# Optimization experiments

Hardware: AMD Instinct MI355X
Metric: run time of the kernel (lower is better)

The kernel has to match this reference:

```python
import jax, jax.numpy as jnp
import numpy as np

K = 16
ITERS = 5
DIST_CHUNK = 8  # feature-chunk size to avoid materializing [B,F,S,S]


def pairwise_l1(x):
    """x: [B, F, S] -> d: [B, S, S], d[b,i,j] = ||x[b,:,i]-x[b,:,j]||_1.
    Computed in feature chunks via scan so peak intermediate is [B,CH,S,S]."""
    B, F, S = x.shape
    xc = x.reshape(B, F // DIST_CHUNK, DIST_CHUNK, S).transpose(1, 0, 2, 3)  # [F/CH,B,CH,S]

    def step(acc, blk):  # blk: [B, CH, S]
        return acc + jnp.abs(blk[:, :, :, None] - blk[:, :, None, :]).sum(axis=1), None

    d, _ = jax.lax.scan(step, jnp.zeros((B, S, S), x.dtype), xc)
    return d


def kmedoids_pool(x, w):
    B, F, S = x.shape
    wm = jnp.mean(w, axis=1)                       # [B,S] per-token attention weight
    d = pairwise_l1(x)                             # [B,S,S]
    _, ctr = jax.lax.top_k(wm, K)                  # [B,K] initial medoids
    dw = d * wm[:, None, :]                        # d[b,i,j]*w[b,j]
    for _ in range(ITERS):
        # distance from every token to each current medoid: [B,S,K]
        i2c = jnp.take_along_axis(d, jnp.broadcast_to(ctr[:, None, :], (B, S, K)), axis=2)
        assign = jnp.argmin(i2c, axis=2)           # [B,S] cluster assignment
        member = jax.nn.one_hot(assign, K, dtype=x.dtype)  # [B,S,K]
        # weighted within-cluster cost for candidate i in cluster k:
        # cost[b,i,k] = sum_j d[b,i,j]*w[b,j]*member[b,j,k]
        cost = jnp.einsum('bij,bjk->bik', dw, member)
        cost = jnp.where(member > 0, cost, jnp.inf)  # medoid must be a member
        ctr = jnp.argmin(cost, axis=1)             # [B,K] new medoids
    idx = jnp.broadcast_to(ctr[:, None, :], (B, F, K))
    return jnp.take_along_axis(x, idx, axis=2)     # [B,F,K]


def setup_inputs() -> dict:
    key = jax.random.key(0)
    kx, kw = jax.random.split(key)
    B, F, S = 8, 256, 1024
    x = jax.random.normal(kx, (B, F, S), dtype=jnp.float32)
    w = jax.random.uniform(kw, (B, S, S), dtype=jnp.float32)
    return {"x": x, "w": w}


def reference(x, w):
    return kmedoids_pool(x, w)
```

## Files before the change

kernel.cpp:

```cpp
#include <hip/hip_runtime.h>
#include <math.h>

#define BB 8
#define FF 256
#define SS 1024
#define KK 16
#define ITERS 5

typedef unsigned long long ull;


#define ICH 8
__global__ void wm_part_kernel(const float* __restrict__ w, float* __restrict__ part) {
    int j = blockIdx.x * 256 + threadIdx.x;
    int ic = blockIdx.y, b = blockIdx.z;
    const float* wp = w + (size_t)b * SS * SS + (size_t)ic * (SS / ICH) * SS + j;
    float s = 0.f;
#pragma unroll 16
    for (int i = 0; i < SS / ICH; ++i) s += wp[(size_t)i * SS];
    part[((size_t)ic * BB + b) * SS + j] = s;
}

#define FCD 8
#define TS 64
#define NT (SS / TS)
__device__ __forceinline__ void async_copy16(const float* g, const float* s) {
    __builtin_amdgcn_global_load_lds((const __attribute__((address_space(1))) void*)g,
                                     (__attribute__((address_space(3))) void*)s, 16, 0, 0);
}

__global__ __launch_bounds__(128, 2) void dist_kernel(const float* __restrict__ x,
                                                      float* __restrict__ d) {
    __shared__ float smem[4096];
    int tid = threadIdx.x;
    int wave = tid >> 6, lane = tid & 63;
    int b = blockIdx.y;
    int w = blockIdx.x * 2 + wave;
    int it = 0, rem = w;
    while (rem >= NT - it) { rem -= NT - it; ++it; }
    int jt = it + rem;
    int i0 = it * TS, j0 = jt * TS;
    const float* xb = x + (size_t)b * FF * SS;
    float* db = d + (size_t)b * SS * SS;
    float* wbase = smem + wave * 2048;
    int ly = lane >> 3, lx = lane & 7;
    int sFl = lane >> 4, sTk = (lane & 15) * 4;

    float acc[8][8] = {};

    auto stage = [&](int c, int h) {
        float* A = wbase + h * 1024;
        const float* base = xb + ((size_t)c * FCD + sFl) * SS;
        async_copy16(base + i0 + sTk, A);
        async_copy16(base + 4 * SS + i0 + sTk, A + 256);
        async_copy16(base + j0 + sTk, A + 512);
        async_copy16(base + 4 * SS + j0 + sTk, A + 768);
    };
    auto compute = [&](int h) {
        const float* A = wbase + h * 1024;
        const float* B = A + 512;
#pragma unroll
        for (int f = 0; f < FCD; ++f) {
            float4 a0 = *(const float4*)(A + f * 64 + ly * 8);
            float4 a1 = *(const float4*)(A + f * 64 + ly * 8 + 4);
            float4 b0 = *(const float4*)(B + f * 64 + lx * 8);
            float4 b1 = *(const float4*)(B + f * 64 + lx * 8 + 4);
            float av[8] = {a0.x, a0.y, a0.z, a0.w, a1.x, a1.y, a1.z, a1.w};
            float bv[8] = {b0.x, b0.y, b0.z, b0.w, b1.x, b1.y, b1.z, b1.w};
#pragma unroll
            for (int r = 0; r < 8; ++r)
#pragma unroll
                for (int c = 0; c < 8; ++c)
                    acc[r][c] += fabsf(av[r] - bv[c]);
        }
    };

    stage(0, 0);
#pragma unroll 1
    for (int k = 0; k < FF / FCD - 1; ++k) {
        asm volatile("s_waitcnt lgkmcnt(0)" ::: "memory");
        stage(k + 1, (k + 1) & 1);
        asm volatile("s_waitcnt vmcnt(4)" ::: "memory");
        compute(k & 1);
    }
    asm volatile("s_waitcnt vmcnt(0)" ::: "memory");
    compute(1);

#pragma unroll
    for (int r = 0; r < 8; ++r) {
        float4 v0 = make_float4(acc[r][0], acc[r][1], acc[r][2], acc[r][3]);
        float4 v1 = make_float4(acc[r][4], acc[r][5], acc[r][6], acc[r][7]);
        float* row = &db[(size_t)(i0 + ly * 8 + r) * SS + j0 + lx * 8];
        *(float4*)row = v0;
        *(float4*)(row + 4) = v1;
    }
    if (it != jt) {
#pragma unroll
        for (int c = 0; c < 8; ++c) {
            float4 v0 = make_float4(acc[0][c], acc[1][c], acc[2][c], acc[3][c]);
            float4 v1 = make_float4(acc[4][c], acc[5][c], acc[6][c], acc[7][c]);
            float* row = &db[(size_t)(j0 + lx * 8 + c) * SS + i0 + ly * 8];
            *(float4*)row = v0;
            *(float4*)(row + 4) = v1;
        }
    }
}

__global__ __launch_bounds__(1024) void topk_assign_kernel(const float* __restrict__ part,
                                                           float* __restrict__ wm,
                                                           const float* __restrict__ d,
                                                           int* __restrict__ assign) {
    int b = blockIdx.x;
    int tid = threadIdx.x;
    int lane = tid & 63, wv = tid >> 6;
    __shared__ ull red[16];
    __shared__ int ctr_s[KK];
    float v = 0.f;
#pragma unroll
    for (int ic = 0; ic < ICH; ++ic) v += part[((size_t)ic * BB + b) * SS + tid];
    v *= (1.0f / SS);
    wm[b * SS + tid] = v;
    ull key = (((ull)__float_as_uint(v)) << 32) | (ull)(0xFFFFFFFFu - (unsigned)tid);
    for (int k = 0; k < KK; ++k) {
        ull kk = key;
#pragma unroll
        for (int off = 32; off; off >>= 1) {
            ull o = __shfl_down(kk, off, 64);
            if (o > kk) kk = o;
        }
        if (lane == 0) red[wv] = kk;
        __syncthreads();
        if (wv == 0) {
            ull k2 = (lane < 16) ? red[lane] : 0ull;
#pragma unroll
            for (int off = 8; off; off >>= 1) {
                ull o = __shfl_down(k2, off, 64);
                if (o > k2) k2 = o;
            }
            if (lane == 0) red[0] = k2;
        }
        __syncthreads();
        ull W = red[0];
        int widx = (int)(0xFFFFFFFFu - (unsigned)(W & 0xFFFFFFFFu));
        if (tid == widx) key = 0;
        if (tid == 0) ctr_s[k] = widx;
        __syncthreads();
    }
    const float* db = d + (size_t)b * SS * SS;
    float bv = INFINITY;
    int bk = 0;
#pragma unroll
    for (int k = 0; k < KK; ++k) {
        float vv = db[(size_t)ctr_s[k] * SS + tid];
        if (vv < bv) { bv = vv; bk = k; }
    }
    assign[b * SS + tid] = bk;
}

#define RPB 16
__global__ __launch_bounds__(256) void cost_kernel(const float* __restrict__ d,
                                                   const float* __restrict__ wm,
                                                   const int* __restrict__ assign,
                                                   float* __restrict__ cost) {
    int b = blockIdx.y;
    int tid = threadIdx.x;
    int lane = tid & 63, wv = tid >> 6;
    __shared__ float wmv[SS];
    __shared__ int asg[SS];
    *(float4*)&wmv[tid * 4] = *(const float4*)&wm[b * SS + tid * 4];
    *(int4*)&asg[tid * 4] = *(const int4*)&assign[b * SS + tid * 4];
    __syncthreads();
    const float* db = d + (size_t)b * SS * SS;
#pragma unroll
    for (int r = 0; r < RPB / 4; ++r) {
        int i = blockIdx.x * RPB + wv * (RPB / 4) + r;
        int my = asg[i];
        const float* drow = db + (size_t)i * SS;
        float s = 0.f;
#pragma unroll
        for (int c = 0; c < SS / 256; ++c) {
            int j = c * 256 + lane * 4;
            float4 dv = *(const float4*)&drow[j];
            float4 wv4 = *(const float4*)&wmv[j];
            int4 a4 = *(const int4*)&asg[j];
            s += (a4.x == my) ? dv.x * wv4.x : 0.f;
            s += (a4.y == my) ? dv.y * wv4.y : 0.f;
            s += (a4.z == my) ? dv.z * wv4.z : 0.f;
            s += (a4.w == my) ? dv.w * wv4.w : 0.f;
        }
#pragma unroll
        for (int off = 32; off; off >>= 1) s += __shfl_down(s, off, 64);
        if (lane == 0) cost[b * SS + i] = s;
    }
}

__global__ __launch_bounds__(1024) void update_assign_kernel(
        const float* __restrict__ d, const float* __restrict__ cost,
        int* __restrict__ assign, const float* __restrict__ x,
        float* __restrict__ out, int last) {
    int b = blockIdx.y;
    int q = blockIdx.x;
    int tid = threadIdx.x;
    int lane = tid & 63, wv = tid >> 6;
    __shared__ float cost_s[SS];
    __shared__ int assign_s[SS];
    __shared__ int ctr_s[KK];
    __shared__ ull pk[4][256];
    cost_s[tid] = cost[b * SS + tid];
    assign_s[tid] = assign[b * SS + tid];
    __syncthreads();
    ull best = ~0ull;
    int k = wv;
    for (int c = 0; c < SS / 64; ++c) {
        int i = c * 64 + lane;
        if (assign_s[i] == k) {
            ull key = (((ull)__float_as_uint(cost_s[i])) << 32) | (unsigned)i;
            if (key < best) best = key;
        }
    }
#pragma unroll
    for (int off = 32; off; off >>= 1) {
        ull o = __shfl_down(best, off, 64);
        if (o < best) best = o;
    }
    if (lane == 0) ctr_s[k] = (best == ~0ull) ? 0 : (int)(best & 0xFFFFFFFFu);
    __syncthreads();
    const float* db = d + (size_t)b * SS * SS;
    if (!last) {
        int tok = q * 256 + (tid & 255);
        int g = tid >> 8;
        ull bk = ~0ull;
#pragma unroll
        for (int kk = 0; kk < 4; ++kk) {
            int k2 = g * 4 + kk;
            float vv = db[(size_t)ctr_s[k2] * SS + tok];
            ull key = (((ull)__float_as_uint(vv)) << 32) | (unsigned)k2;
            if (key < bk) bk = key;
        }
        pk[g][tid & 255] = bk;
        __syncthreads();
        if (tid < 256) {
            ull m = pk[0][tid];
            if (pk[1][tid] < m) m = pk[1][tid];
            if (pk[2][tid] < m) m = pk[2][tid];
            if (pk[3][tid] < m) m = pk[3][tid];
            assign[b * SS + q * 256 + tid] = (int)(m & 0xFFFFFFFFu);
        }
    } else {
        int e = q * 1024 + tid;
        int f = e / KK, k2 = e % KK;
        out[((size_t)b * FF + f) * KK + k2] = x[((size_t)b * FF + f) * SS + ctr_s[k2]];
    }
}

extern "C" void kernel_launch(void* const* d_in, const int* in_sizes, int n_in,
                              void* d_out, int out_size, void* d_ws, size_t ws_size,
                              hipStream_t stream) {
    const float* x = (const float*)d_in[0];
    const float* w = (const float*)d_in[1];
    float* out = (float*)d_out;

    char* ws = (char*)d_ws;
    float* d = (float*)ws;
    size_t off = (size_t)BB * SS * SS * sizeof(float);
    float* wm = (float*)(ws + off);   off += (size_t)BB * SS * sizeof(float);
    int* assign = (int*)(ws + off);   off += (size_t)BB * SS * sizeof(int);
    float* cost = (float*)(ws + off); off += (size_t)BB * SS * sizeof(float);
    float* part = (float*)(ws + off);

    dist_kernel<<<dim3(68, BB), 128, 0, stream>>>(x, d);
    wm_part_kernel<<<dim3(SS / 256, ICH, BB), 256, 0, stream>>>(w, part);
    topk_assign_kernel<<<BB, 1024, 0, stream>>>(part, wm, d, assign);
    for (int itr = 0; itr < ITERS; ++itr) {
        cost_kernel<<<dim3(SS / RPB, BB), 256, 0, stream>>>(d, wm, assign, cost);
        update_assign_kernel<<<dim3(4, BB), 1024, 0, stream>>>(d, cost, assign, x, out,
                                                               itr == ITERS - 1 ? 1 : 0);
    }
}
```

Baseline: 282.5 us.

## Split each 64x64 distance tile across two waves sharing staged LDS

Each block now computes one 64x64 upper-triangular tile, with its two waves each handling 32 rows and sharing the staged feature chunks. Previously each wave owned its own tile. Each thread keeps a 4x8 accumulator instead of 8x8, and launch bounds rise to 4 blocks per CU with half the shared memory, aiming for more occupancy and a finer grid of 136x8 blocks. In exchange it adds block-wide s_barrier synchronisation on every chunk and lowers the arithmetic per LDS load.

After: 252.6 us. -10.6%, faster.

```diff
diff --git a/kernel.cpp b/kernel.cpp
--- a/kernel.cpp
+++ b/kernel.cpp
@@ -29,46 +29,43 @@
                                      (__attribute__((address_space(3))) void*)s, 16, 0, 0);
 }
 
-__global__ __launch_bounds__(128, 2) void dist_kernel(const float* __restrict__ x,
+__global__ __launch_bounds__(128, 4) void dist_kernel(const float* __restrict__ x,
                                                       float* __restrict__ d) {
-    __shared__ float smem[4096];
+    __shared__ float smem[2048];
     int tid = threadIdx.x;
     int wave = tid >> 6, lane = tid & 63;
     int b = blockIdx.y;
-    int w = blockIdx.x * 2 + wave;
+    int w = blockIdx.x;
     int it = 0, rem = w;
     while (rem >= NT - it) { rem -= NT - it; ++it; }
     int jt = it + rem;
     int i0 = it * TS, j0 = jt * TS;
     const float* xb = x + (size_t)b * FF * SS;
     float* db = d + (size_t)b * SS * SS;
-    float* wbase = smem + wave * 2048;
-    int ly = lane >> 3, lx = lane & 7;
-    int sFl = lane >> 4, sTk = (lane & 15) * 4;
-
-    float acc[8][8] = {};
+    int rl = wave * 32 + (lane >> 3) * 4;
+    int cl = (lane & 7) * 8;
+    int sF = tid >> 4, sT = (tid & 15) * 4;
+
+    float acc[4][8] = {};
 
     auto stage = [&](int c, int h) {
-        float* A = wbase + h * 1024;
-        const float* base = xb + ((size_t)c * FCD + sFl) * SS;
-        async_copy16(base + i0 + sTk, A);
-        async_copy16(base + 4 * SS + i0 + sTk, A + 256);
-        async_copy16(base + j0 + sTk, A + 512);
-        async_copy16(base + 4 * SS + j0 + sTk, A + 768);
+        float* A = smem + h * 1024 + wave * 256;
+        const float* base = xb + ((size_t)c * FCD + sF) * SS + sT;
+        async_copy16(base + i0, A);
+        async_copy16(base + j0, A + 512);
     };
     auto compute = [&](int h) {
-        const float* A = wbase + h * 1024;
+        const float* A = smem + h * 1024;
         const float* B = A + 512;
 #pragma unroll
         for (int f = 0; f < FCD; ++f) {
-            float4 a0 = *(const float4*)(A + f * 64 + ly * 8);
-            float4 a1 = *(const float4*)(A + f * 64 + ly * 8 + 4);
-            float4 b0 = *(const float4*)(B + f * 64 + lx * 8);
-            float4 b1 = *(const float4*)(B + f * 64 + lx * 8 + 4);
-            float av[8] = {a0.x, a0.y, a0.z, a0.w, a1.x, a1.y, a1.z, a1.w};
+            float4 a4 = *(const float4*)(A + f * 64 + rl);
+            float4 b0 = *(const float4*)(B + f * 64 + cl);
+            float4 b1 = *(const float4*)(B + f * 64 + cl + 4);
+            float av[4] = {a4.x, a4.y, a4.z, a4.w};
             float bv[8] = {b0.x, b0.y, b0.z, b0.w, b1.x, b1.y, b1.z, b1.w};
 #pragma unroll
-            for (int r = 0; r < 8; ++r)
+            for (int r = 0; r < 4; ++r)
 #pragma unroll
                 for (int c = 0; c < 8; ++c)
                     acc[r][c] += fabsf(av[r] - bv[c]);
@@ -78,30 +75,29 @@
     stage(0, 0);
 #pragma unroll 1
     for (int k = 0; k < FF / FCD - 1; ++k) {
-        asm volatile("s_waitcnt lgkmcnt(0)" ::: "memory");
+        asm volatile("s_barrier" ::: "memory");
         stage(k + 1, (k + 1) & 1);
-        asm volatile("s_waitcnt vmcnt(4)" ::: "memory");
+        asm volatile("s_waitcnt vmcnt(2)" ::: "memory");
+        asm volatile("s_barrier" ::: "memory");
         compute(k & 1);
     }
     asm volatile("s_waitcnt vmcnt(0)" ::: "memory");
+    asm volatile("s_barrier" ::: "memory");
     compute(1);
 
 #pragma unroll
-    for (int r = 0; r < 8; ++r) {
+    for (int r = 0; r < 4; ++r) {
         float4 v0 = make_float4(acc[r][0], acc[r][1], acc[r][2], acc[r][3]);
         float4 v1 = make_float4(acc[r][4], acc[r][5], acc[r][6], acc[r][7]);
-        float* row = &db[(size_t)(i0 + ly * 8 + r) * SS + j0 + lx * 8];
+        float* row = &db[(size_t)(i0 + rl + r) * SS + j0 + cl];
         *(float4*)row = v0;
         *(float4*)(row + 4) = v1;
     }
     if (it != jt) {
 #pragma unroll
         for (int c = 0; c < 8; ++c) {
-            float4 v0 = make_float4(acc[0][c], acc[1][c], acc[2][c], acc[3][c]);
-            float4 v1 = make_float4(acc[4][c], acc[5][c], acc[6][c], acc[7][c]);
-            float* row = &db[(size_t)(j0 + lx * 8 + c) * SS + i0 + ly * 8];
-            *(float4*)row = v0;
-            *(float4*)(row + 4) = v1;
+            float4 v = make_float4(acc[0][c], acc[1][c], acc[2][c], acc[3][c]);
+            *(float4*)&db[(size_t)(j0 + cl + c) * SS + i0 + rl] = v;
         }
     }
 }
@@ -268,7 +264,7 @@
     float* cost = (float*)(ws + off); off += (size_t)BB * SS * sizeof(float);
     float* part = (float*)(ws + off);
 
-    dist_kernel<<<dim3(68, BB), 128, 0, stream>>>(x, d);
+    dist_kernel<<<dim3(136, BB), 128, 0, stream>>>(x, d);
     wm_part_kernel<<<dim3(SS / 256, ICH, BB), 256, 0, stream>>>(w, part);
     topk_assign_kernel<<<BB, 1024, 0, stream>>>(part, wm, d, assign);
     for (int itr = 0; itr < ITERS; ++itr) {
```

## Shrink distance tiles to 32x32 per wave with 4-deep async LDS pipeline

Applied to the files above, without the earlier changes.

Halves the distance tile per wave from 64x64 to 32x32, so each lane holds a 4x4 accumulator instead of 8x8, and raises the launch-bounds occupancy hint from 2 to 4. The grid grows from 68 to 264 blocks per batch to cover the 528 upper-triangle tiles. Staging moves from a double buffer to a 4-slot ring with two chunks prefetched ahead. The aim is more waves in flight and better load balance across CUs, paid for by lower arithmetic intensity per LDS load and more global reads of x.

Result: faster. 228.2 us (-19.2%).

```diff
diff --git a/kernel.cpp b/kernel.cpp
--- a/kernel.cpp
+++ b/kernel.cpp
@@ -22,14 +22,14 @@
 }
 
 #define FCD 8
-#define TS 64
+#define TS 32
 #define NT (SS / TS)
 __device__ __forceinline__ void async_copy16(const float* g, const float* s) {
     __builtin_amdgcn_global_load_lds((const __attribute__((address_space(1))) void*)g,
                                      (__attribute__((address_space(3))) void*)s, 16, 0, 0);
 }
 
-__global__ __launch_bounds__(128, 2) void dist_kernel(const float* __restrict__ x,
+__global__ __launch_bounds__(128, 4) void dist_kernel(const float* __restrict__ x,
                                                       float* __restrict__ d) {
     __shared__ float smem[4096];
     int tid = threadIdx.x;
@@ -44,64 +44,56 @@
     float* db = d + (size_t)b * SS * SS;
     float* wbase = smem + wave * 2048;
     int ly = lane >> 3, lx = lane & 7;
-    int sFl = lane >> 4, sTk = (lane & 15) * 4;
-
-    float acc[8][8] = {};
-
-    auto stage = [&](int c, int h) {
-        float* A = wbase + h * 1024;
+    int sFl = lane >> 3, sTk = (lane & 7) * 4;
+
+    float acc[4][4] = {};
+
+    auto stage = [&](int c) {
+        float* A = wbase + (c & 3) * 512;
         const float* base = xb + ((size_t)c * FCD + sFl) * SS;
         async_copy16(base + i0 + sTk, A);
-        async_copy16(base + 4 * SS + i0 + sTk, A + 256);
-        async_copy16(base + j0 + sTk, A + 512);
-        async_copy16(base + 4 * SS + j0 + sTk, A + 768);
+        async_copy16(base + j0 + sTk, A + 256);
     };
-    auto compute = [&](int h) {
-        const float* A = wbase + h * 1024;
-        const float* B = A + 512;
+    auto compute = [&](int c) {
+        const float* A = wbase + (c & 3) * 512;
+        const float* B = A + 256;
 #pragma unroll
         for (int f = 0; f < FCD; ++f) {
-            float4 a0 = *(const float4*)(A + f * 64 + ly * 8);
-            float4 a1 = *(const float4*)(A + f * 64 + ly * 8 + 4);
-            float4 b0 = *(const float4*)(B + f * 64 + lx * 8);
-            float4 b1 = *(const float4*)(B + f * 64 + lx * 8 + 4);
-            float av[8] = {a0.x, a0.y, a0.z, a0.w, a1.x, a1.y, a1.z, a1.w};
-            float bv[8] = {b0.x, b0.y, b0.z, b0.w, b1.x, b1.y, b1.z, b1.w};
-#pragma unroll
-            for (int r = 0; r < 8; ++r)
-#pragma unroll
-                for (int c = 0; c < 8; ++c)
-                    acc[r][c] += fabsf(av[r] - bv[c]);
+            float4 a = *(const float4*)(A + f * 32 + ly * 4);
+            float4 bb = *(const float4*)(B + f * 32 + lx * 4);
+            float av[4] = {a.x, a.y, a.z, a.w};
+            float bv[4] = {bb.x, bb.y, bb.z, bb.w};
+#pragma unroll
+            for (int r = 0; r < 4; ++r)
+#pragma unroll
+                for (int cc = 0; cc < 4; ++cc)
+                    acc[r][cc] += fabsf(av[r] - bv[cc]);
         }
     };
 
-    stage(0, 0);
+    stage(0); stage(1);
 #pragma unroll 1
-    for (int k = 0; k < FF / FCD - 1; ++k) {
+    for (int c = 0; c < FF / FCD - 2; ++c) {
         asm volatile("s_waitcnt lgkmcnt(0)" ::: "memory");
-        stage(k + 1, (k + 1) & 1);
+        stage(c + 2);
         asm volatile("s_waitcnt vmcnt(4)" ::: "memory");
-        compute(k & 1);
-    }
+        compute(c);
+    }
+    asm volatile("s_waitcnt vmcnt(2)" ::: "memory");
+    compute(30);
     asm volatile("s_waitcnt vmcnt(0)" ::: "memory");
-    compute(1);
-
-#pragma unroll
-    for (int r = 0; r < 8; ++r) {
-        float4 v0 = make_float4(acc[r][0], acc[r][1], acc[r][2], acc[r][3]);
-        float4 v1 = make_float4(acc[r][4], acc[r][5], acc[r][6], acc[r][7]);
-        float* row = &db[(size_t)(i0 + ly * 8 + r) * SS + j0 + lx * 8];
-        *(float4*)row = v0;
-        *(float4*)(row + 4) = v1;
+    compute(31);
+
+#pragma unroll
+    for (int r = 0; r < 4; ++r) {
+        float4 v = make_float4(acc[r][0], acc[r][1], acc[r][2], acc[r][3]);
+        *(float4*)&db[(size_t)(i0 + ly * 4 + r) * SS + j0 + lx * 4] = v;
     }
     if (it != jt) {
 #pragma unroll
-        for (int c = 0; c < 8; ++c) {
-            float4 v0 = make_float4(acc[0][c], acc[1][c], acc[2][c], acc[3][c]);
-            float4 v1 = make_float4(acc[4][c], acc[5][c], acc[6][c], acc[7][c]);
-            float* row = &db[(size_t)(j0 + lx * 8 + c) * SS + i0 + ly * 8];
-            *(float4*)row = v0;
-            *(float4*)(row + 4) = v1;
+        for (int c = 0; c < 4; ++c) {
+            float4 v = make_float4(acc[0][c], acc[1][c], acc[2][c], acc[3][c]);
+            *(float4*)&db[(size_t)(j0 + lx * 4 + c) * SS + i0 + ly * 4] = v;
         }
     }
 }
@@ -268,7 +260,7 @@
     float* cost = (float*)(ws + off); off += (size_t)BB * SS * sizeof(float);
     float* part = (float*)(ws + off);
 
-    dist_kernel<<<dim3(68, BB), 128, 0, stream>>>(x, d);
+    dist_kernel<<<dim3(264, BB), 128, 0, stream>>>(x, d);
     wm_part_kernel<<<dim3(SS / 256, ICH, BB), 256, 0, stream>>>(w, part);
     topk_assign_kernel<<<BB, 1024, 0, stream>>>(part, wm, d, assign);
     for (int itr = 0; itr < ITERS; ++itr) {
```
